# Kernel optimization log

Hardware: AMD Instinct MI355X
Metric: run time of the kernel (lower is better)

## Reference

```python
import jax, jax.numpy as jnp
import numpy as np

NUM_ITERATIONS = 3
EPS = 1e-12  # matches torch F.normalize default eps


def setup_inputs() -> dict:
    key = jax.random.key(0)
    k1, k2 = jax.random.split(key)
    B, IN_CAPS, IN_LEN = 64, 1152, 8
    OUT_CAPS, OUT_LEN = 64, 16
    x = jax.random.normal(k1, (B, IN_CAPS, IN_LEN), dtype=jnp.float32)
    # xavier_uniform over (out_caps, out_len, in_len): fan_in=in_len, fan_out=out_len
    limit = float(np.sqrt(6.0 / (IN_LEN + OUT_LEN)))
    weight = jax.random.uniform(k2, (OUT_CAPS, OUT_LEN, IN_LEN), dtype=jnp.float32,
                                minval=-limit, maxval=limit)
    return {"x": x, "weight": weight}


def reference(x, weight):
    # priors[b,o,n,l] = sum_i weight[o,l,i] * x[b,n,i]  -> [B, out_caps, in_caps, out_len]
    priors = jnp.einsum('oli,bni->bonl', weight, x)
    # k-means routing, similarity='dot', squash=False (module defaults)
    out = jnp.mean(priors, axis=-2, keepdims=True)  # [B, O, 1, L] initial centroid
    probs = None
    for _ in range(NUM_ITERATIONS):
        norm = jnp.linalg.norm(out, axis=-1, keepdims=True)
        out_n = out / jnp.maximum(norm, EPS)  # F.normalize(output, dim=-1)
        logits = jnp.sum(priors * out_n, axis=-1, keepdims=True)  # [B, O, N, 1]
        probs = jax.nn.softmax(logits, axis=-2)  # softmax over in_capsules
        out = jnp.sum(probs * priors, axis=-2, keepdims=True)  # [B, O, 1, L]
    # squash=False -> return raw centroid
    return out.squeeze(-2), probs.squeeze(-1)  # [B, O, L], [B, O, N]
```

## Files before the change

kernel.cpp:

```cpp
#include <hip/hip_runtime.h>
#include <math.h>


#define NCAPS 1152
#define ILEN  8
#define OCAPS 64
#define OLEN  16
#define T     128
#define RPT   9
#define NW    2
#define NITER 3

#define BSTAGE(OFF, H)                                              \
    {                                                               \
        const bool up = (lane & (OFF)) != 0;                        \
        _Pragma("unroll")                                           \
        for (int j = 0; j < (H); ++j) {                             \
            float keep = up ? s[(H) + j] : s[j];                    \
            float send = up ? s[j] : s[(H) + j];                    \
            s[j] = keep + __shfl_xor(send, (OFF), 64);              \
        }                                                           \
    }

__global__ __launch_bounds__(T, 4) void caps_kernel(const float* __restrict__ x,
                                                    const float* __restrict__ w,
                                                    float* __restrict__ dout,
                                                    int probs_base) {
    const int tid  = threadIdx.x;
    const int lane = tid & 63;
    const int wid  = tid >> 6;
    const int o = blockIdx.x & (OCAPS - 1);
    const int b = blockIdx.x >> 6;

    __shared__ __align__(16) float ws[OLEN * ILEN];
    __shared__ float red[NW][ILEN];
    __shared__ float redz[NW];
    __shared__ float ylds[ILEN];

    ws[tid] = w[o * OLEN * ILEN + tid];

    const float* xb = x + (size_t)b * NCAPS * ILEN;
    float xr[RPT][ILEN];
    #pragma unroll
    for (int k = 0; k < RPT; ++k) {
        const float4* q = (const float4*)(xb + (size_t)(tid + k * T) * ILEN);
        float4 a = q[0], c = q[1];
        xr[k][0] = a.x; xr[k][1] = a.y; xr[k][2] = a.z; xr[k][3] = a.w;
        xr[k][4] = c.x; xr[k][5] = c.y; xr[k][6] = c.z; xr[k][7] = c.w;
    }

    float e[RPT];

    #pragma unroll
    for (int it = 0; it <= NITER; ++it) {
        if (it > 0) {
            float yv[ILEN];
            #pragma unroll
            for (int i = 0; i < ILEN; ++i) yv[i] = ylds[i];
            #pragma unroll
            for (int k = 0; k < RPT; ++k) {
                float lg = xr[k][0] * yv[0];
                #pragma unroll
                for (int i = 1; i < ILEN; ++i) lg = fmaf(xr[k][i], yv[i], lg);
                e[k] = __expf(lg);
            }
        } else {
            #pragma unroll
            for (int k = 0; k < RPT; ++k) e[k] = 1.0f;
        }

        float s[ILEN];
        #pragma unroll
        for (int i = 0; i < ILEN; ++i) {
            float acc = e[0] * xr[0][i];
            #pragma unroll
            for (int k = 1; k < RPT; ++k) acc = fmaf(e[k], xr[k][i], acc);
            s[i] = acc;
        }
        float z = e[0];
        #pragma unroll
        for (int k = 1; k < RPT; ++k) z += e[k];

        BSTAGE(1, 4)
        BSTAGE(2, 2)
        BSTAGE(4, 1)
        float s0 = s[0];
        s0 += __shfl_xor(s0, 8, 64);
        s0 += __shfl_xor(s0, 16, 64);
        s0 += __shfl_xor(s0, 32, 64);
        #pragma unroll
        for (int off = 1; off < 64; off <<= 1) z += __shfl_xor(z, off, 64);

        if (lane < 8) {
            const int c = ((lane & 1) << 2) | (lane & 2) | ((lane & 4) >> 2);
            red[wid][c] = s0;
        }
        if (lane == 0) redz[wid] = z;
        __syncthreads();

        const float zt   = redz[0] + redz[1];
        const float zinv = 1.0f / zt;

        if (it < NITER) {
            if (wid == 0) {
                float sv = (lane < 8) ? (red[0][lane] + red[1][lane]) : 0.0f;
                float sb[ILEN];
                #pragma unroll
                for (int i = 0; i < ILEN; ++i) sb[i] = __shfl(sv, i, 64);
                const int l16 = lane & 15;
                const float4 w0 = *(const float4*)&ws[l16 * ILEN];
                const float4 w1 = *(const float4*)&ws[l16 * ILEN + 4];
                float outl = w0.x * sb[0];
                outl = fmaf(w0.y, sb[1], outl);
                outl = fmaf(w0.z, sb[2], outl);
                outl = fmaf(w0.w, sb[3], outl);
                outl = fmaf(w1.x, sb[4], outl);
                outl = fmaf(w1.y, sb[5], outl);
                outl = fmaf(w1.z, sb[6], outl);
                outl = fmaf(w1.w, sb[7], outl);
                outl *= zinv;
                float n2 = outl * outl;
                n2 += __shfl_xor(n2, 1, 64);
                n2 += __shfl_xor(n2, 2, 64);
                n2 += __shfl_xor(n2, 4, 64);
                n2 += __shfl_xor(n2, 8, 64);
                const float inv = 1.0f / fmaxf(sqrtf(n2), 1e-12f);
                float ob[OLEN];
                #pragma unroll
                for (int l = 0; l < OLEN; ++l) ob[l] = __shfl(outl, l, 64);
                const int i8 = lane & 7;
                float yv = ws[i8] * ob[0];
                #pragma unroll
                for (int l = 1; l < OLEN; ++l) yv = fmaf(ws[l * ILEN + i8], ob[l], yv);
                if (lane < 8) ylds[lane] = yv * inv;
            }
            __syncthreads();
        } else {
            if (wid == 0) {
                float sv = (lane < 8) ? (red[0][lane] + red[1][lane]) : 0.0f;
                float sb[ILEN];
                #pragma unroll
                for (int i = 0; i < ILEN; ++i) sb[i] = __shfl(sv, i, 64);
                const int l16 = lane & 15;
                const float4 w0 = *(const float4*)&ws[l16 * ILEN];
                const float4 w1 = *(const float4*)&ws[l16 * ILEN + 4];
                float outl = w0.x * sb[0];
                outl = fmaf(w0.y, sb[1], outl);
                outl = fmaf(w0.z, sb[2], outl);
                outl = fmaf(w0.w, sb[3], outl);
                outl = fmaf(w1.x, sb[4], outl);
                outl = fmaf(w1.y, sb[5], outl);
                outl = fmaf(w1.z, sb[6], outl);
                outl = fmaf(w1.w, sb[7], outl);
                outl *= zinv;
                if (lane < OLEN) dout[(size_t)blockIdx.x * OLEN + lane] = outl;
            }
            float* probp = dout + (size_t)probs_base + (size_t)blockIdx.x * NCAPS;
            #pragma unroll
            for (int k = 0; k < RPT; ++k) probp[tid + k * T] = e[k] * zinv;
        }
    }
}

extern "C" void kernel_launch(void* const* d_in, const int* in_sizes, int n_in,
                              void* d_out, int out_size, void* d_ws, size_t ws_size,
                              hipStream_t stream) {
    const float* x = (const float*)d_in[0];
    const float* w = (const float*)d_in[1];
    float* out = (float*)d_out;
    const int Bv = in_sizes[0] / (NCAPS * ILEN);
    const int nblocks = Bv * OCAPS;
    const int probs_base = nblocks * OLEN;
    caps_kernel<<<dim3(nblocks), dim3(T), 0, stream>>>(x, w, out, probs_base);
}
```

Baseline: 78.93 us.

## Process four output capsules per block to reuse register-resident x across capsules

Each block now handles four output capsules for one batch instead of one, keeping x in registers once and reusing it for all four routing computations. Block size grows to 192 threads with 6 rows each, and the final reduction/normalisation is spread across two waves (one half-wave per capsule). The first iteration skips the exp/weighting work by summing x directly with a constant normaliser. This cuts redundant global loads of x and block launch overhead, at the cost of more registers per thread and fewer blocks (1024 vs 4096).

```diff
diff --git a/kernel.cpp b/kernel.cpp
--- a/kernel.cpp
+++ b/kernel.cpp
@@ -6,9 +6,11 @@
 #define ILEN  8
 #define OCAPS 64
 #define OLEN  16
-#define T     128
-#define RPT   9
-#define NW    2
+#define T     192
+#define NW    3
+#define RPT   6
+#define G     4
+#define NBLK_O (OCAPS / G)
 #define NITER 3
 
 #define BSTAGE(OFF, H)                                              \
@@ -22,24 +24,44 @@
         }                                                           \
     }
 
-__global__ __launch_bounds__(T, 4) void caps_kernel(const float* __restrict__ x,
+__device__ __forceinline__ float vec8_wave_reduce(float* s, int lane) {
+    BSTAGE(1, 4)
+    BSTAGE(2, 2)
+    BSTAGE(4, 1)
+    float s0 = s[0];
+    s0 += __shfl_xor(s0, 8, 64);
+    s0 += __shfl_xor(s0, 16, 64);
+    s0 += __shfl_xor(s0, 32, 64);
+    return s0;
+}
+
+__global__ __launch_bounds__(T, 3) void caps_kernel(const float* __restrict__ x,
                                                     const float* __restrict__ w,
                                                     float* __restrict__ dout,
                                                     int probs_base) {
     const int tid  = threadIdx.x;
     const int lane = tid & 63;
     const int wid  = tid >> 6;
-    const int o = blockIdx.x & (OCAPS - 1);
-    const int b = blockIdx.x >> 6;
-
-    __shared__ __align__(16) float ws[OLEN * ILEN];
-    __shared__ float red[NW][ILEN];
-    __shared__ float redz[NW];
-    __shared__ float ylds[ILEN];
-
-    ws[tid] = w[o * OLEN * ILEN + tid];
-
-    const float* xb = x + (size_t)b * NCAPS * ILEN;
+    const int og = blockIdx.x & (NBLK_O - 1);
+    const int b  = blockIdx.x >> 4;
+    const int o0 = og * G;
+
+    __shared__ __align__(16) float ws[G][OLEN * ILEN];
+    __shared__ float red[NW][G][ILEN];
+    __shared__ float redz[NW][G];
+    __shared__ float ylds[G][ILEN];
+
+    {
+        const float* wsrc = w + (size_t)o0 * (OLEN * ILEN);
+        float* wdst = &ws[0][0];
+        #pragma unroll
+        for (int j = 0; j < 3; ++j) {
+            const int idx = tid + j * T;
+            if (idx < G * OLEN * ILEN) wdst[idx] = wsrc[idx];
+        }
+    }
+
+    const float* xb = x + (size_t)b * (NCAPS * ILEN);
     float xr[RPT][ILEN];
     #pragma unroll
     for (int k = 0; k < RPT; ++k) {
@@ -49,67 +71,85 @@
         xr[k][4] = c.x; xr[k][5] = c.y; xr[k][6] = c.z; xr[k][7] = c.w;
     }
 
-    float e[RPT];
-
     #pragma unroll
     for (int it = 0; it <= NITER; ++it) {
-        if (it > 0) {
-            float yv[ILEN];
-            #pragma unroll
-            for (int i = 0; i < ILEN; ++i) yv[i] = ylds[i];
-            #pragma unroll
-            for (int k = 0; k < RPT; ++k) {
-                float lg = xr[k][0] * yv[0];
-                #pragma unroll
-                for (int i = 1; i < ILEN; ++i) lg = fmaf(xr[k][i], yv[i], lg);
-                e[k] = __expf(lg);
+        float e[G][RPT];
+        if (it == 0) {
+            float s[ILEN];
+            #pragma unroll
+            for (int i = 0; i < ILEN; ++i) {
+                float acc = xr[0][i];
+                #pragma unroll
+                for (int k = 1; k < RPT; ++k) acc += xr[k][i];
+                s[i] = acc;
+            }
+            const float s0 = vec8_wave_reduce(s, lane);
+            if (lane < 8) {
+                const int c = ((lane & 1) << 2) | (lane & 2) | ((lane & 4) >> 2);
+                #pragma unroll
+                for (int g = 0; g < G; ++g) red[wid][g][c] = s0;
+            }
+            if (lane == 0) {
+                #pragma unroll
+                for (int g = 0; g < G; ++g) redz[wid][g] = (float)NCAPS / (float)NW;
             }
         } else {
             #pragma unroll
-            for (int k = 0; k < RPT; ++k) e[k] = 1.0f;
+            for (int g = 0; g < G; ++g) {
+                float yv[ILEN];
+                #pragma unroll
+                for (int i = 0; i < ILEN; ++i) yv[i] = ylds[g][i];
+                #pragma unroll
+                for (int k = 0; k < RPT; ++k) {
+                    float lg = xr[k][0] * yv[0];
+                    #pragma unroll
+                    for (int i = 1; i < ILEN; ++i) lg = fmaf(xr[k][i], yv[i], lg);
+                    e[g][k] = __expf(lg);
+                }
+            }
+            float s0g[G], zg[G];
+            #pragma unroll
+            for (int g = 0; g < G; ++g) {
+                float s[ILEN];
+                #pragma unroll
+                for (int i = 0; i < ILEN; ++i) {
+                    float acc = e[g][0] * xr[0][i];
+                    #pragma unroll
+                    for (int k = 1; k < RPT; ++k) acc = fmaf(e[g][k], xr[k][i], acc);
+                    s[i] = acc;
+                }
+                float z = e[g][0];
+                #pragma unroll
+                for (int k = 1; k < RPT; ++k) z += e[g][k];
+                s0g[g] = vec8_wave_reduce(s, lane);
+                #pragma unroll
+                for (int off = 1; off < 64; off <<= 1) z += __shfl_xor(z, off, 64);
+                zg[g] = z;
+            }
+            if (lane < 8) {
+                const int c = ((lane & 1) << 2) | (lane & 2) | ((lane & 4) >> 2);
+                #pragma unroll
+                for (int g = 0; g < G; ++g) red[wid][g][c] = s0g[g];
+            }
+            if (lane == 0) {
+                #pragma unroll
+                for (int g = 0; g < G; ++g) redz[wid][g] = zg[g];
+            }
         }
-
-        float s[ILEN];
-        #pragma unroll
-        for (int i = 0; i < ILEN; ++i) {
-            float acc = e[0] * xr[0][i];
-            #pragma unroll
-            for (int k = 1; k < RPT; ++k) acc = fmaf(e[k], xr[k][i], acc);
-            s[i] = acc;
-        }
-        float z = e[0];
-        #pragma unroll
-        for (int k = 1; k < RPT; ++k) z += e[k];
-
-        BSTAGE(1, 4)
-        BSTAGE(2, 2)
-        BSTAGE(4, 1)
-        float s0 = s[0];
-        s0 += __shfl_xor(s0, 8, 64);
-        s0 += __shfl_xor(s0, 16, 64);
-        s0 += __shfl_xor(s0, 32, 64);
-        #pragma unroll
-        for (int off = 1; off < 64; off <<= 1) z += __shfl_xor(z, off, 64);
-
-        if (lane < 8) {
-            const int c = ((lane & 1) << 2) | (lane & 2) | ((lane & 4) >> 2);
-            red[wid][c] = s0;
-        }
-        if (lane == 0) redz[wid] = z;
         __syncthreads();
 
-        const float zt   = redz[0] + redz[1];
-        const float zinv = 1.0f / zt;
-
         if (it < NITER) {
-            if (wid == 0) {
-                float sv = (lane < 8) ? (red[0][lane] + red[1][lane]) : 0.0f;
+            if (wid < 2) {
+                const int ge  = wid * 2 + (lane >> 5);
+                const int sub = lane & 31;
+                const int l   = sub & 15;
                 float sb[ILEN];
                 #pragma unroll
-                for (int i = 0; i < ILEN; ++i) sb[i] = __shfl(sv, i, 64);
-                const int l16 = lane & 15;
-                const float4 w0 = *(const float4*)&ws[l16 * ILEN];
-                const float4 w1 = *(const float4*)&ws[l16 * ILEN + 4];
+                for (int i = 0; i < ILEN; ++i)
+                    sb[i] = red[0][ge][i] + red[1][ge][i] + red[2][ge][i];
+                const float zinv = 1.0f / (redz[0][ge] + redz[1][ge] + redz[2][ge]);
+                const float4 w0 = *(const float4*)&ws[ge][l * ILEN];
+                const float4 w1 = *(const float4*)&ws[ge][l * ILEN + 4];
                 float outl = w0.x * sb[0];
                 outl = fmaf(w0.y, sb[1], outl);
                 outl = fmaf(w0.z, sb[2], outl);
@@ -126,24 +166,29 @@
                 n2 += __shfl_xor(n2, 8, 64);
                 const float inv = 1.0f / fmaxf(sqrtf(n2), 1e-12f);
                 float ob[OLEN];
-                #pragma unroll
-                for (int l = 0; l < OLEN; ++l) ob[l] = __shfl(outl, l, 64);
-                const int i8 = lane & 7;
-                float yv = ws[i8] * ob[0];
-                #pragma unroll
-                for (int l = 1; l < OLEN; ++l) yv = fmaf(ws[l * ILEN + i8], ob[l], yv);
-                if (lane < 8) ylds[lane] = yv * inv;
+                const int gb = lane & 48;
+                #pragma unroll
+                for (int l2 = 0; l2 < OLEN; ++l2) ob[l2] = __shfl(outl, gb + l2, 64);
+                const int i8 = sub & 7;
+                float yv = ws[ge][i8] * ob[0];
+                #pragma unroll
+                for (int l2 = 1; l2 < OLEN; ++l2)
+                    yv = fmaf(ws[ge][l2 * ILEN + i8], ob[l2], yv);
+                if (sub < 8) ylds[ge][i8] = yv * inv;
             }
             __syncthreads();
         } else {
-            if (wid == 0) {
-                float sv = (lane < 8) ? (red[0][lane] + red[1][lane]) : 0.0f;
+            if (wid < 2) {
+                const int ge  = wid * 2 + (lane >> 5);
+                const int sub = lane & 31;
+                const int l   = sub & 15;
                 float sb[ILEN];
                 #pragma unroll
-                for (int i = 0; i < ILEN; ++i) sb[i] = __shfl(sv, i, 64);
-                const int l16 = lane & 15;
-                const float4 w0 = *(const float4*)&ws[l16 * ILEN];
-                const float4 w1 = *(const float4*)&ws[l16 * ILEN + 4];
+                for (int i = 0; i < ILEN; ++i)
+                    sb[i] = red[0][ge][i] + red[1][ge][i] + red[2][ge][i];
+                const float zinv = 1.0f / (redz[0][ge] + redz[1][ge] + redz[2][ge]);
+                const float4 w0 = *(const float4*)&ws[ge][l * ILEN];
+                const float4 w1 = *(const float4*)&ws[ge][l * ILEN + 4];
                 float outl = w0.x * sb[0];
                 outl = fmaf(w0.y, sb[1], outl);
                 outl = fmaf(w0.z, sb[2], outl);
@@ -153,11 +198,20 @@
                 outl = fmaf(w1.z, sb[6], outl);
                 outl = fmaf(w1.w, sb[7], outl);
                 outl *= zinv;
-                if (lane < OLEN) dout[(size_t)blockIdx.x * OLEN + lane] = outl;
-            }
-            float* probp = dout + (size_t)probs_base + (size_t)blockIdx.x * NCAPS;
-            #pragma unroll
-            for (int k = 0; k < RPT; ++k) probp[tid + k * T] = e[k] * zinv;
+                if (sub < 16)
+                    dout[((size_t)(b * OCAPS + o0 + ge)) * OLEN + l] = outl;
+            }
+            float pinv[G];
+            #pragma unroll
+            for (int g = 0; g < G; ++g)
+                pinv[g] = 1.0f / (redz[0][g] + redz[1][g] + redz[2][g]);
+            #pragma unroll
+            for (int g = 0; g < G; ++g) {
+                float* pp = dout + (size_t)probs_base
+                                 + (size_t)(b * OCAPS + o0 + g) * NCAPS;
+                #pragma unroll
+                for (int k = 0; k < RPT; ++k) pp[tid + k * T] = e[g][k] * pinv[g];
+            }
         }
     }
 }
@@ -169,7 +223,7 @@
     const float* w = (const float*)d_in[1];
     float* out = (float*)d_out;
     const int Bv = in_sizes[0] / (NCAPS * ILEN);
-    const int nblocks = Bv * OCAPS;
-    const int probs_base = nblocks * OLEN;
+    const int nblocks = Bv * NBLK_O;
+    const int probs_base = Bv * OCAPS * OLEN;
     caps_kernel<<<dim3(nblocks), dim3(T), 0, stream>>>(x, w, out, probs_base);
 }
```

Result: no change. 79.20 us (+0.3%).

## Use DPP wave reductions and redundant per-wave centroid math to drop a barrier

Applied to the files above, without the earlier changes.

Replaces the shuffle-based butterfly reductions with DPP row/wave reductions and readlane broadcasts. Both waves now redundantly compute the centroid, normalization and projected vector in registers, with weights held in registers. This removes the second __syncthreads per iteration and the LDS staging of weights and y. Per-iteration LDS slots avoid write-after-read hazards. Each wave now reduces all 8 components separately instead of using the transpose-style butterfly, which adds some extra VALU/DPP work.

```diff
diff --git a/kernel.cpp b/kernel.cpp
--- a/kernel.cpp
+++ b/kernel.cpp
@@ -7,20 +7,39 @@
 #define OCAPS 64
 #define OLEN  16
 #define T     128
+#define NW    2
 #define RPT   9
-#define NW    2
 #define NITER 3
 
-#define BSTAGE(OFF, H)                                              \
-    {                                                               \
-        const bool up = (lane & (OFF)) != 0;                        \
-        _Pragma("unroll")                                           \
-        for (int j = 0; j < (H); ++j) {                             \
-            float keep = up ? s[(H) + j] : s[j];                    \
-            float send = up ? s[j] : s[(H) + j];                    \
-            s[j] = keep + __shfl_xor(send, (OFF), 64);              \
-        }                                                           \
-    }
+template<int CTRL>
+__device__ __forceinline__ float dpp_mov0(float x) {
+    int xi = __builtin_bit_cast(int, x);
+    int r  = __builtin_amdgcn_update_dpp(0, xi, CTRL, 0xf, 0xf, true);
+    return __builtin_bit_cast(float, r);
+}
+
+__device__ __forceinline__ float wave_sum63(float v) {
+    v += dpp_mov0<0x111>(v);
+    v += dpp_mov0<0x112>(v);
+    v += dpp_mov0<0x114>(v);
+    v += dpp_mov0<0x118>(v);
+    v += dpp_mov0<0x142>(v);
+    v += dpp_mov0<0x143>(v);
+    return v;
+}
+
+__device__ __forceinline__ float row16_sum(float v) {
+    v += dpp_mov0<0x111>(v);
+    v += dpp_mov0<0x112>(v);
+    v += dpp_mov0<0x114>(v);
+    v += dpp_mov0<0x118>(v);
+    return v;
+}
+
+__device__ __forceinline__ float bcast_lane(float v, int lane) {
+    return __builtin_bit_cast(float,
+        __builtin_amdgcn_readlane(__builtin_bit_cast(int, v), lane));
+}
 
 __global__ __launch_bounds__(T, 4) void caps_kernel(const float* __restrict__ x,
                                                     const float* __restrict__ w,
@@ -29,17 +48,21 @@
     const int tid  = threadIdx.x;
     const int lane = tid & 63;
     const int wid  = tid >> 6;
+    const int l16  = lane & 15;
     const int o = blockIdx.x & (OCAPS - 1);
     const int b = blockIdx.x >> 6;
 
-    __shared__ __align__(16) float ws[OLEN * ILEN];
-    __shared__ float red[NW][ILEN];
-    __shared__ float redz[NW];
-    __shared__ float ylds[ILEN];
+    __shared__ __align__(16) float red[NITER + 1][NW][12];
 
-    ws[tid] = w[o * OLEN * ILEN + tid];
+    float wreg[ILEN];
+    {
+        const float4* wp = (const float4*)(w + ((size_t)o * OLEN + l16) * ILEN);
+        float4 a = wp[0], c = wp[1];
+        wreg[0] = a.x; wreg[1] = a.y; wreg[2] = a.z; wreg[3] = a.w;
+        wreg[4] = c.x; wreg[5] = c.y; wreg[6] = c.z; wreg[7] = c.w;
+    }
 
-    const float* xb = x + (size_t)b * NCAPS * ILEN;
+    const float* xb = x + (size_t)b * (NCAPS * ILEN);
     float xr[RPT][ILEN];
     #pragma unroll
     for (int k = 0; k < RPT; ++k) {
@@ -50,114 +73,81 @@
     }
 
     float e[RPT];
+    float ysg[ILEN];
 
     #pragma unroll
     for (int it = 0; it <= NITER; ++it) {
-        if (it > 0) {
-            float yv[ILEN];
+        float s[ILEN];
+        float z = 0.0f;
+        if (it == 0) {
             #pragma unroll
-            for (int i = 0; i < ILEN; ++i) yv[i] = ylds[i];
-            #pragma unroll
-            for (int k = 0; k < RPT; ++k) {
-                float lg = xr[k][0] * yv[0];
+            for (int i = 0; i < ILEN; ++i) {
+                float acc = xr[0][i];
                 #pragma unroll
-                for (int i = 1; i < ILEN; ++i) lg = fmaf(xr[k][i], yv[i], lg);
-                e[k] = __expf(lg);
+                for (int k = 1; k < RPT; ++k) acc += xr[k][i];
+                s[i] = acc;
             }
         } else {
             #pragma unroll
-            for (int k = 0; k < RPT; ++k) e[k] = 1.0f;
+            for (int k = 0; k < RPT; ++k) {
+                float lg = xr[k][0] * ysg[0];
+                #pragma unroll
+                for (int i = 1; i < ILEN; ++i) lg = fmaf(xr[k][i], ysg[i], lg);
+                e[k] = __expf(lg);
+            }
+            #pragma unroll
+            for (int i = 0; i < ILEN; ++i) {
+                float acc = e[0] * xr[0][i];
+                #pragma unroll
+                for (int k = 1; k < RPT; ++k) acc = fmaf(e[k], xr[k][i], acc);
+                s[i] = acc;
+            }
+            z = e[0];
+            #pragma unroll
+            for (int k = 1; k < RPT; ++k) z += e[k];
         }
 
-        float s[ILEN];
         #pragma unroll
-        for (int i = 0; i < ILEN; ++i) {
-            float acc = e[0] * xr[0][i];
-            #pragma unroll
-            for (int k = 1; k < RPT; ++k) acc = fmaf(e[k], xr[k][i], acc);
-            s[i] = acc;
+        for (int i = 0; i < ILEN; ++i) s[i] = wave_sum63(s[i]);
+        if (it > 0) z = wave_sum63(z);
+
+        if (lane == 63) {
+            *(float4*)&red[it][wid][0] = make_float4(s[0], s[1], s[2], s[3]);
+            *(float4*)&red[it][wid][4] = make_float4(s[4], s[5], s[6], s[7]);
+            red[it][wid][8] = z;
         }
-        float z = e[0];
-        #pragma unroll
-        for (int k = 1; k < RPT; ++k) z += e[k];
-
-        BSTAGE(1, 4)
-        BSTAGE(2, 2)
-        BSTAGE(4, 1)
-        float s0 = s[0];
-        s0 += __shfl_xor(s0, 8, 64);
-        s0 += __shfl_xor(s0, 16, 64);
-        s0 += __shfl_xor(s0, 32, 64);
-        #pragma unroll
-        for (int off = 1; off < 64; off <<= 1) z += __shfl_xor(z, off, 64);
-
-        if (lane < 8) {
-            const int c = ((lane & 1) << 2) | (lane & 2) | ((lane & 4) >> 2);
-            red[wid][c] = s0;
-        }
-        if (lane == 0) redz[wid] = z;
         __syncthreads();
 
-        const float zt   = redz[0] + redz[1];
-        const float zinv = 1.0f / zt;
+        float4 a0 = *(const float4*)&red[it][0][0];
+        float4 a1 = *(const float4*)&red[it][0][4];
+        float4 b0 = *(const float4*)&red[it][1][0];
+        float4 b1 = *(const float4*)&red[it][1][4];
+        float sc[ILEN];
+        sc[0] = a0.x + b0.x; sc[1] = a0.y + b0.y; sc[2] = a0.z + b0.z; sc[3] = a0.w + b0.w;
+        sc[4] = a1.x + b1.x; sc[5] = a1.y + b1.y; sc[6] = a1.z + b1.z; sc[7] = a1.w + b1.w;
+        const float zc   = (it == 0) ? (float)NCAPS : (red[it][0][8] + red[it][1][8]);
+        const float zinv = 1.0f / zc;
+
+        float ol = wreg[0] * sc[0];
+        #pragma unroll
+        for (int i = 1; i < ILEN; ++i) ol = fmaf(wreg[i], sc[i], ol);
+        ol *= zinv;
 
         if (it < NITER) {
-            if (wid == 0) {
-                float sv = (lane < 8) ? (red[0][lane] + red[1][lane]) : 0.0f;
-                float sb[ILEN];
-                #pragma unroll
-                for (int i = 0; i < ILEN; ++i) sb[i] = __shfl(sv, i, 64);
-                const int l16 = lane & 15;
-                const float4 w0 = *(const float4*)&ws[l16 * ILEN];
-                const float4 w1 = *(const float4*)&ws[l16 * ILEN + 4];
-                float outl = w0.x * sb[0];
-                outl = fmaf(w0.y, sb[1], outl);
-                outl = fmaf(w0.z, sb[2], outl);
-                outl = fmaf(w0.w, sb[3], outl);
-                outl = fmaf(w1.x, sb[4], outl);
-                outl = fmaf(w1.y, sb[5], outl);
-                outl = fmaf(w1.z, sb[6], outl);
-                outl = fmaf(w1.w, sb[7], outl);
-                outl *= zinv;
-                float n2 = outl * outl;
-                n2 += __shfl_xor(n2, 1, 64);
-                n2 += __shfl_xor(n2, 2, 64);
-                n2 += __shfl_xor(n2, 4, 64);
-                n2 += __shfl_xor(n2, 8, 64);
-                const float inv = 1.0f / fmaxf(sqrtf(n2), 1e-12f);
-                float ob[OLEN];
-                #pragma unroll
-                for (int l = 0; l < OLEN; ++l) ob[l] = __shfl(outl, l, 64);
-                const int i8 = lane & 7;
-                float yv = ws[i8] * ob[0];
-                #pragma unroll
-                for (int l = 1; l < OLEN; ++l) yv = fmaf(ws[l * ILEN + i8], ob[l], yv);
-                if (lane < 8) ylds[lane] = yv * inv;
+            float n2 = row16_sum(ol * ol);
+            n2 = bcast_lane(n2, 15);
+            const float inv = 1.0f / fmaxf(sqrtf(n2), 1e-12f);
+            const float oh = ol * inv;
+            #pragma unroll
+            for (int i = 0; i < ILEN; ++i) {
+                float t = row16_sum(wreg[i] * oh);
+                ysg[i] = bcast_lane(t, 15);
             }
-            __syncthreads();
         } else {
-            if (wid == 0) {
-                float sv = (lane < 8) ? (red[0][lane] + red[1][lane]) : 0.0f;
-                float sb[ILEN];
-                #pragma unroll
-                for (int i = 0; i < ILEN; ++i) sb[i] = __shfl(sv, i, 64);
-                const int l16 = lane & 15;
-                const float4 w0 = *(const float4*)&ws[l16 * ILEN];
-                const float4 w1 = *(const float4*)&ws[l16 * ILEN + 4];
-                float outl = w0.x * sb[0];
-                outl = fmaf(w0.y, sb[1], outl);
-                outl = fmaf(w0.z, sb[2], outl);
-                outl = fmaf(w0.w, sb[3], outl);
-                outl = fmaf(w1.x, sb[4], outl);
-                outl = fmaf(w1.y, sb[5], outl);
-                outl = fmaf(w1.z, sb[6], outl);
-                outl = fmaf(w1.w, sb[7], outl);
-                outl *= zinv;
-                if (lane < OLEN) dout[(size_t)blockIdx.x * OLEN + lane] = outl;
-            }
-            float* probp = dout + (size_t)probs_base + (size_t)blockIdx.x * NCAPS;
+            if (tid < OLEN) dout[(size_t)blockIdx.x * OLEN + tid] = ol;
+            float* pp = dout + (size_t)probs_base + (size_t)blockIdx.x * NCAPS;
             #pragma unroll
-            for (int k = 0; k < RPT; ++k) probp[tid + k * T] = e[k] * zinv;
+            for (int k = 0; k < RPT; ++k) pp[tid + k * T] = e[k] * zinv;
         }
     }
 }
```

Result: slower. 80.92 us (+2.5%).
